# Performance work log

Hardware: AMD Instinct MI355X
Metric: run time of the kernel (lower is better)

Reference implementation:

```python
import jax, jax.numpy as jnp
import numpy as np

V = 25   # NTU joints
NE = 5   # number of hyper-edge types


def setup_inputs() -> dict:
    key = jax.random.key(0)
    ks = jax.random.split(key, 8)
    N, C, T = 64, 12, 300
    x = jax.random.normal(ks[0], (N, C, T, V), dtype=jnp.float32)
    # binary incidence matrices [V, E] with E == V, as in the NTU hyper-edge tables
    hs = [jax.random.bernoulli(ks[1 + i], 0.2, (V, V)).astype(jnp.float32) for i in range(NE)]
    in_ch, out_ch = 3, 64
    w_mlp = jax.random.normal(ks[6], (out_ch, in_ch * NE), dtype=jnp.float32) * (1.0 / np.sqrt(in_ch * NE))
    b_mlp = jnp.zeros((out_ch,), dtype=jnp.float32)
    return {"x": x, "h_local": hs[0], "h_center": hs[1], "h_figl": hs[2],
            "h_figr": hs[3], "h_hand": hs[4], "w_mlp": w_mlp, "b_mlp": b_mlp}


def _normalized_aggregate(w, h):
    # w: [N, T, E], h: [V, E] (E == V)
    degree_v = jnp.einsum('ve,bte->btv', h, w)
    # pow(d, -0.5): inf at d==0 and nan at d<0 are both zeroed in the original
    dv_pos = degree_v > 0
    degree_v = jnp.where(dv_pos, jax.lax.rsqrt(jnp.where(dv_pos, degree_v, 1.0)), 0.0)
    degree_e = jnp.sum(h, axis=0)                      # [E]
    de_nz = degree_e != 0
    degree_e = jnp.where(de_nz, 1.0 / jnp.where(de_nz, degree_e, 1.0), 0.0)
    # fused dh * w * degree_e chain: [N, T, V, E]
    dhwb = degree_v[..., None] * h[None, None] * w[:, :, None, :] * degree_e
    dhwbht = jnp.einsum('btve,ue->btvu', dhwb, h)      # [N, T, V, V]
    return dhwbht * degree_v[:, :, None, :]


def reference(x, h_local, h_center, h_figl, h_figr, h_hand, w_mlp, b_mlp):
    ws = (x[:, 6], x[:, 7], x[:, 9], x[:, 10], x[:, 11])
    hs = (h_local, h_center, h_figl, h_figr, h_hand)
    hwh_cat = jnp.concatenate([_normalized_aggregate(w, h) for w, h in zip(ws, hs)], axis=-2)  # [N,T,5V,V]
    feat = x[:, :3]                                    # [N, 3, T, V]
    N, C, T, Vv = feat.shape
    support = jnp.einsum('btvu,bctu->bctv', hwh_cat, feat)          # [N, C, T, 5V]
    support = support.reshape(N, C, T, NE, Vv).transpose(0, 3, 1, 2, 4).reshape(N, NE * C, T, Vv)
    out = jnp.einsum('oi,bitv->botv', w_mlp, support) + b_mlp[None, :, None, None]
    return jax.nn.relu(out)
```

## Files before the change

### kernel.cpp

```cpp
#include <hip/hip_runtime.h>

#define NE  5
#define V   25
#define NT  300
#define NC  12
#define CO  64
#define WPB 4
#define GX  38
#define WOFF 384

typedef float f4 __attribute__((ext_vector_type(4)));
typedef float f2 __attribute__((ext_vector_type(2)));

#define WSYNC() do { asm volatile("s_waitcnt lgkmcnt(0)" ::: "memory"); \
                     __builtin_amdgcn_sched_barrier(0); } while (0)

__device__ __forceinline__ float hsel(unsigned m, int e, float w) {
    int s = ((int)(m << (31 - e))) >> 31;
    return __int_as_float(__float_as_int(w) & s);
}

#define ODV  0
#define OFP  250
#define OE_  1000
#define OFT  1250
#define OB_  1400
#define OST  1000
#define SCRF 2152

__global__ void setup_kernel(const float* __restrict__ h0, const float* __restrict__ h1,
                             const float* __restrict__ h2, const float* __restrict__ h3,
                             const float* __restrict__ h4,
                             const float* __restrict__ wmlp, const float* __restrict__ bmlp,
                             unsigned* __restrict__ ws) {
    int tid = threadIdx.x;
    float* wsf = (float*)ws;
    if (tid < 125) {
        int i = tid / 25, v = tid % 25;
        const float* hp = (i==0)?h0:(i==1)?h1:(i==2)?h2:(i==3)?h3:h4;
        unsigned m = 0;
        for (int e = 0; e < V; ++e) if (hp[v*V + e] != 0.f) m |= (1u << e);
        ws[tid] = m;
    } else if (tid < 250) {
        int idx = tid - 125, i = idx / 25, e = idx % 25;
        const float* hp = (i==0)?h0:(i==1)?h1:(i==2)?h2:(i==3)?h3:h4;
        unsigned m = 0; float s = 0.f;
        for (int u = 0; u < V; ++u) {
            float hv = hp[u*V + e];
            s += hv;
            if (hv != 0.f) m |= (1u << u);
        }
        ws[tid] = m;
        wsf[125 + tid] = (s != 0.f) ? __fdiv_rn(1.f, s) : 0.f;
    }
    for (int q = tid; q < CO*16; q += 384) {
        int o = q >> 4, k = q & 15;
        wsf[WOFF + q] = (k < 15) ? wmlp[o*15 + k] : bmlp[o];
    }
}

__global__ __launch_bounds__(256, 4) void hyper_main(
    const float* __restrict__ x,
    const unsigned* __restrict__ ws,
    float* __restrict__ out)
{
    __shared__ unsigned RM[125];
    __shared__ unsigned CM[125];
    __shared__ float    DE[125];
    __shared__ __align__(16) float SCR[WPB][SCRF];

    const int tid  = threadIdx.x;
    const int lane = tid & 63;
    const int wid  = tid >> 6;
    const int b    = blockIdx.y;
    const float* wsf = (const float*)ws;

    if (tid < 125) {
        RM[tid] = ws[tid];
    } else if (tid < 250) {
        CM[tid - 125] = ws[tid];
        DE[tid - 125] = wsf[tid + 125];
    }
    __syncthreads();

    const int pp = blockIdx.x * WPB + wid;
    if (pp >= NT/2) return;

    float* S = SCR[wid];

    float pf[7]; int lo[7];
    #pragma unroll
    for (int r = 0; r < 7; ++r) {
        int q  = r*64 + lane;
        int qq = (q < 400) ? q : 0;
        int tt = qq / 200, rr = qq % 200, ch = rr / 25, e = rr % 25;
        int xc = (ch < 5) ? (ch + 6 + (ch >= 2 ? 1 : 0)) : (ch - 5);
        lo[r] = ((ch < 5) ? (OE_ + tt*125 + ch*25) : (OFT + tt*75 + (ch-5)*25)) + e;
        pf[r] = x[((size_t)(b*NC + xc)*NT + (2*pp + tt))*V + e];
    }
    #pragma unroll
    for (int r = 0; r < 6; ++r) S[lo[r]] = pf[r];
    if (lane < 16) S[lo[6]] = pf[6];
    WSYNC();

    #pragma unroll
    for (int r = 0; r < 4; ++r) {
        int idx = r*64 + lane;
        if (idx < 250) {
            int tt  = (idx >= 125) ? 1 : 0;
            int rem = idx - (tt ? 125 : 0);
            int i = rem / 25, v = rem % 25;
            unsigned m = RM[rem];
            const float* wi = S + OE_ + tt*125 + i*25;
            float L0 = 0.f, L1 = 0.f, L2 = 0.f, L3 = 0.f;
            unsigned mm;
            mm = m & 0x00111111u;
            while (mm) { int e = __builtin_ctz(mm); mm &= mm-1; L0 = __fadd_rn(L0, wi[e]); }
            mm = m & 0x00222222u;
            while (mm) { int e = __builtin_ctz(mm); mm &= mm-1; L1 = __fadd_rn(L1, wi[e]); }
            mm = m & 0x00444444u;
            while (mm) { int e = __builtin_ctz(mm); mm &= mm-1; L2 = __fadd_rn(L2, wi[e]); }
            mm = m & 0x00888888u;
            while (mm) { int e = __builtin_ctz(mm); mm &= mm-1; L3 = __fadd_rn(L3, wi[e]); }
            float s = __fadd_rn(__fadd_rn(L0, L1), __fadd_rn(L2, L3));
            s = __fadd_rn(s, hsel(m, 24, wi[24]));
            float dvv = (s > 0.f) ? (float)(1.0 / sqrt((double)s)) : 0.f;
            S[ODV + tt*125 + i*25 + v] = dvv;
            float f0  = S[OFT + tt*75 +  0 + v];
            float f1  = S[OFT + tt*75 + 25 + v];
            float f2v = S[OFT + tt*75 + 50 + v];
            S[OB_ + tt*375 +   0 + i*25 + v] = dvv * f0;
            S[OB_ + tt*375 + 125 + i*25 + v] = dvv * f1;
            S[OB_ + tt*375 + 250 + i*25 + v] = dvv * f2v;
        }
    }
    WSYNC();

    #pragma unroll
    for (int r = 0; r < 4; ++r) {
        int idx = r*64 + lane;
        if (idx < 250) {
            int tt  = (idx >= 125) ? 1 : 0;
            int rem = idx - (tt ? 125 : 0);
            int i = rem / 25, e = rem % 25;
            unsigned m = CM[rem];
            const float* bp = S + OB_ + tt*375 + i*25;
            float a0 = 0.f, a1 = 0.f, a2 = 0.f;
            while (m) {
                int u = __builtin_ctz(m); m &= m - 1;
                a0 += bp[u]; a1 += bp[125 + u]; a2 += bp[250 + u];
            }
            float gg = S[OE_ + tt*125 + i*25 + e] * DE[rem];
            S[OFP + tt*375 + (i*3+0)*25 + e] = a0 * gg;
            S[OFP + tt*375 + (i*3+1)*25 + e] = a1 * gg;
            S[OFP + tt*375 + (i*3+2)*25 + e] = a2 * gg;
        }
    }
    WSYNC();

    #pragma unroll
    for (int r = 0; r < 4; ++r) {
        int idx = r*64 + lane;
        if (idx < 250) {
            int tt  = (idx >= 125) ? 1 : 0;
            int rem = idx - (tt ? 125 : 0);
            int i = rem / 25, v = rem % 25;
            unsigned m = RM[rem];
            const float* fp = S + OFP + tt*375 + i*3*25;
            float a0 = 0.f, a1 = 0.f, a2 = 0.f;
            while (m) {
                int e = __builtin_ctz(m); m &= m - 1;
                a0 += fp[e]; a1 += fp[25 + e]; a2 += fp[50 + e];
            }
            float dd = S[ODV + tt*125 + i*25 + v];
            float* st = S + OST + (tt*25 + v)*20 + i*3;
            st[0] = a0 * dd; st[1] = a1 * dd; st[2] = a2 * dd;
        }
    }
    WSYNC();

    if (lane < 50) {
        const float* st = S + OST + lane*20;
        f4 s0 = *(const f4*)(st+0), s1 = *(const f4*)(st+4),
           s2 = *(const f4*)(st+8), s3 = *(const f4*)(st+12);
        float* ob = out + (size_t)b*CO*7500 + (size_t)pp*50 + lane;
        const f4* wq = (const f4*)(wsf + WOFF);
        #pragma unroll 4
        for (int o = 0; o < CO; ++o) {
            f4 c0 = wq[4*o+0], c1 = wq[4*o+1], c2 = wq[4*o+2], c3 = wq[4*o+3];
            f2 acc = (f2){c3.w, 0.f};
            acc += (f2){c0.x, c0.y} * (f2){s0.x, s0.y};
            acc += (f2){c0.z, c0.w} * (f2){s0.z, s0.w};
            acc += (f2){c1.x, c1.y} * (f2){s1.x, s1.y};
            acc += (f2){c1.z, c1.w} * (f2){s1.z, s1.w};
            acc += (f2){c2.x, c2.y} * (f2){s2.x, s2.y};
            acc += (f2){c2.z, c2.w} * (f2){s2.z, s2.w};
            acc += (f2){c3.x, c3.y} * (f2){s3.x, s3.y};
            float res = acc.x + __fmaf_rn(c3.z, s3.z, acc.y);
            __builtin_nontemporal_store(fmaxf(res, 0.f), ob + (size_t)o*7500);
        }
    }
}

extern "C" void kernel_launch(void* const* d_in, const int* in_sizes, int n_in,
                              void* d_out, int out_size, void* d_ws, size_t ws_size,
                              hipStream_t stream) {
    const float* x    = (const float*)d_in[0];
    const float* h0   = (const float*)d_in[1];
    const float* h1   = (const float*)d_in[2];
    const float* h2   = (const float*)d_in[3];
    const float* h3   = (const float*)d_in[4];
    const float* h4   = (const float*)d_in[5];
    const float* wmlp = (const float*)d_in[6];
    const float* bmlp = (const float*)d_in[7];
    float* out = (float*)d_out;
    unsigned* wsm = (unsigned*)d_ws;

    setup_kernel<<<dim3(1,1,1), dim3(384,1,1), 0, stream>>>(
        h0, h1, h2, h3, h4, wmlp, bmlp, wsm);
    hyper_main<<<dim3(GX, 64, 1), dim3(256,1,1), 0, stream>>>(x, wsm, out);
}
```

Before: 83.35 us.

## Split fused kernel into aggregation and MLP kernels via workspace staging

The single fused kernel becomes two. The aggregation kernel now handles one timestep per wavefront instead of two, which halves shared memory per wave and raises the occupancy target to 8. It writes the 15-channel support, padded to 16, into a global staging buffer. A separate MLP kernel reads that buffer with all 256 threads active and writes the 64 output channels. Before, only 50 of 64 lanes did the MLP and store phase. The cost is an extra global write and read of the staged support (about 30 MB) plus one more kernel launch.

```diff
diff --git a/kernel.cpp b/kernel.cpp
--- a/kernel.cpp
+++ b/kernel.cpp
@@ -5,9 +5,8 @@
 #define NT  300
 #define NC  12
 #define CO  64
-#define WPB 4
-#define GX  38
 #define WOFF 384
+#define STOFF 2048
 
 typedef float f4 __attribute__((ext_vector_type(4)));
 typedef float f2 __attribute__((ext_vector_type(2)));
@@ -21,12 +20,12 @@
 }
 
 #define ODV  0
-#define OFP  250
-#define OE_  1000
-#define OFT  1250
-#define OB_  1400
-#define OST  1000
-#define SCRF 2152
+#define OFP  125
+#define OE_  500
+#define OFT  625
+#define OB_  700
+#define OST  500
+#define SCRF 1088
 
 __global__ void setup_kernel(const float* __restrict__ h0, const float* __restrict__ h1,
                              const float* __restrict__ h2, const float* __restrict__ h3,
@@ -59,15 +58,15 @@
     }
 }
 
-__global__ __launch_bounds__(256, 4) void hyper_main(
+__global__ __launch_bounds__(256, 8) void hyper_agg(
     const float* __restrict__ x,
     const unsigned* __restrict__ ws,
-    float* __restrict__ out)
+    float* __restrict__ wsf_out)
 {
     __shared__ unsigned RM[125];
     __shared__ unsigned CM[125];
     __shared__ float    DE[125];
-    __shared__ __align__(16) float SCR[WPB][SCRF];
+    __shared__ __align__(16) float SCR[4][SCRF];
 
     const int tid  = threadIdx.x;
     const int lane = tid & 63;
@@ -83,35 +82,28 @@
     }
     __syncthreads();
 
-    const int pp = blockIdx.x * WPB + wid;
-    if (pp >= NT/2) return;
-
+    const int t = blockIdx.x * 4 + wid;
     float* S = SCR[wid];
 
-    float pf[7]; int lo[7];
-    #pragma unroll
-    for (int r = 0; r < 7; ++r) {
-        int q  = r*64 + lane;
-        int qq = (q < 400) ? q : 0;
-        int tt = qq / 200, rr = qq % 200, ch = rr / 25, e = rr % 25;
-        int xc = (ch < 5) ? (ch + 6 + (ch >= 2 ? 1 : 0)) : (ch - 5);
-        lo[r] = ((ch < 5) ? (OE_ + tt*125 + ch*25) : (OFT + tt*75 + (ch-5)*25)) + e;
-        pf[r] = x[((size_t)(b*NC + xc)*NT + (2*pp + tt))*V + e];
-    }
-    #pragma unroll
-    for (int r = 0; r < 6; ++r) S[lo[r]] = pf[r];
-    if (lane < 16) S[lo[6]] = pf[6];
-    WSYNC();
-
     #pragma unroll
     for (int r = 0; r < 4; ++r) {
+        int q = r*64 + lane;
+        if (q < 200) {
+            int ch = q / 25, e = q % 25;
+            int xc = (ch < 5) ? (ch + 6 + (ch >= 2 ? 1 : 0)) : (ch - 5);
+            int o = (ch < 5) ? (OE_ + ch*25 + e) : (OFT + (ch-5)*25 + e);
+            S[o] = x[((size_t)(b*NC + xc)*NT + t)*V + e];
+        }
+    }
+    WSYNC();
+
+    #pragma unroll
+    for (int r = 0; r < 2; ++r) {
         int idx = r*64 + lane;
-        if (idx < 250) {
-            int tt  = (idx >= 125) ? 1 : 0;
-            int rem = idx - (tt ? 125 : 0);
-            int i = rem / 25, v = rem % 25;
-            unsigned m = RM[rem];
-            const float* wi = S + OE_ + tt*125 + i*25;
+        if (idx < 125) {
+            int i = idx / 25, v = idx % 25;
+            unsigned m = RM[idx];
+            const float* wi = S + OE_ + i*25;
             float L0 = 0.f, L1 = 0.f, L2 = 0.f, L3 = 0.f;
             unsigned mm;
             mm = m & 0x00111111u;
@@ -125,80 +117,93 @@
             float s = __fadd_rn(__fadd_rn(L0, L1), __fadd_rn(L2, L3));
             s = __fadd_rn(s, hsel(m, 24, wi[24]));
             float dvv = (s > 0.f) ? (float)(1.0 / sqrt((double)s)) : 0.f;
-            S[ODV + tt*125 + i*25 + v] = dvv;
-            float f0  = S[OFT + tt*75 +  0 + v];
-            float f1  = S[OFT + tt*75 + 25 + v];
-            float f2v = S[OFT + tt*75 + 50 + v];
-            S[OB_ + tt*375 +   0 + i*25 + v] = dvv * f0;
-            S[OB_ + tt*375 + 125 + i*25 + v] = dvv * f1;
-            S[OB_ + tt*375 + 250 + i*25 + v] = dvv * f2v;
-        }
-    }
-    WSYNC();
-
-    #pragma unroll
-    for (int r = 0; r < 4; ++r) {
+            S[ODV + i*25 + v] = dvv;
+            S[OB_ +   0 + i*25 + v] = dvv * S[OFT +  0 + v];
+            S[OB_ + 125 + i*25 + v] = dvv * S[OFT + 25 + v];
+            S[OB_ + 250 + i*25 + v] = dvv * S[OFT + 50 + v];
+        }
+    }
+    WSYNC();
+
+    #pragma unroll
+    for (int r = 0; r < 2; ++r) {
         int idx = r*64 + lane;
-        if (idx < 250) {
-            int tt  = (idx >= 125) ? 1 : 0;
-            int rem = idx - (tt ? 125 : 0);
-            int i = rem / 25, e = rem % 25;
-            unsigned m = CM[rem];
-            const float* bp = S + OB_ + tt*375 + i*25;
+        if (idx < 125) {
+            int i = idx / 25, e = idx % 25;
+            unsigned m = CM[idx];
+            const float* bp = S + OB_ + i*25;
             float a0 = 0.f, a1 = 0.f, a2 = 0.f;
             while (m) {
                 int u = __builtin_ctz(m); m &= m - 1;
                 a0 += bp[u]; a1 += bp[125 + u]; a2 += bp[250 + u];
             }
-            float gg = S[OE_ + tt*125 + i*25 + e] * DE[rem];
-            S[OFP + tt*375 + (i*3+0)*25 + e] = a0 * gg;
-            S[OFP + tt*375 + (i*3+1)*25 + e] = a1 * gg;
-            S[OFP + tt*375 + (i*3+2)*25 + e] = a2 * gg;
-        }
-    }
-    WSYNC();
-
-    #pragma unroll
-    for (int r = 0; r < 4; ++r) {
+            float gg = S[OE_ + i*25 + e] * DE[idx];
+            S[OFP + (i*3+0)*25 + e] = a0 * gg;
+            S[OFP + (i*3+1)*25 + e] = a1 * gg;
+            S[OFP + (i*3+2)*25 + e] = a2 * gg;
+        }
+    }
+    WSYNC();
+
+    #pragma unroll
+    for (int r = 0; r < 3; ++r) {
         int idx = r*64 + lane;
-        if (idx < 250) {
-            int tt  = (idx >= 125) ? 1 : 0;
-            int rem = idx - (tt ? 125 : 0);
-            int i = rem / 25, v = rem % 25;
-            unsigned m = RM[rem];
-            const float* fp = S + OFP + tt*375 + i*3*25;
+        if (idx < 125) {
+            int i = idx / 25, v = idx % 25;
+            unsigned m = RM[idx];
+            const float* fp = S + OFP + i*3*25;
             float a0 = 0.f, a1 = 0.f, a2 = 0.f;
             while (m) {
                 int e = __builtin_ctz(m); m &= m - 1;
                 a0 += fp[e]; a1 += fp[25 + e]; a2 += fp[50 + e];
             }
-            float dd = S[ODV + tt*125 + i*25 + v];
-            float* st = S + OST + (tt*25 + v)*20 + i*3;
+            float dd = S[ODV + i*25 + v];
+            float* st = S + OST + v*16 + i*3;
             st[0] = a0 * dd; st[1] = a1 * dd; st[2] = a2 * dd;
-        }
-    }
-    WSYNC();
-
-    if (lane < 50) {
-        const float* st = S + OST + lane*20;
-        f4 s0 = *(const f4*)(st+0), s1 = *(const f4*)(st+4),
-           s2 = *(const f4*)(st+8), s3 = *(const f4*)(st+12);
-        float* ob = out + (size_t)b*CO*7500 + (size_t)pp*50 + lane;
-        const f4* wq = (const f4*)(wsf + WOFF);
-        #pragma unroll 4
-        for (int o = 0; o < CO; ++o) {
-            f4 c0 = wq[4*o+0], c1 = wq[4*o+1], c2 = wq[4*o+2], c3 = wq[4*o+3];
-            f2 acc = (f2){c3.w, 0.f};
-            acc += (f2){c0.x, c0.y} * (f2){s0.x, s0.y};
-            acc += (f2){c0.z, c0.w} * (f2){s0.z, s0.w};
-            acc += (f2){c1.x, c1.y} * (f2){s1.x, s1.y};
-            acc += (f2){c1.z, c1.w} * (f2){s1.z, s1.w};
-            acc += (f2){c2.x, c2.y} * (f2){s2.x, s2.y};
-            acc += (f2){c2.z, c2.w} * (f2){s2.z, s2.w};
-            acc += (f2){c3.x, c3.y} * (f2){s3.x, s3.y};
-            float res = acc.x + __fmaf_rn(c3.z, s3.z, acc.y);
-            __builtin_nontemporal_store(fmaxf(res, 0.f), ob + (size_t)o*7500);
-        }
+        } else if (idx < 150) {
+            S[OST + (idx - 125)*16 + 15] = 0.f;
+        }
+    }
+    WSYNC();
+
+    if (lane < 25) {
+        const f4* sr = (const f4*)(S + OST + lane*16);
+        f4 r0 = sr[0], r1 = sr[1], r2 = sr[2], r3 = sr[3];
+        f4* stg = (f4*)(wsf_out + STOFF) + ((size_t)b*7500 + t*25 + lane)*4;
+        __builtin_nontemporal_store(r0, stg + 0);
+        __builtin_nontemporal_store(r1, stg + 1);
+        __builtin_nontemporal_store(r2, stg + 2);
+        __builtin_nontemporal_store(r3, stg + 3);
+    }
+}
+
+__global__ __launch_bounds__(256, 8) void hyper_mlp(
+    const unsigned* __restrict__ ws,
+    float* __restrict__ out)
+{
+    const float* wsf = (const float*)ws;
+    const int p = blockIdx.x * 256 + threadIdx.x;
+    if (p >= 7500) return;
+    const int b = blockIdx.y;
+
+    const f4* sp = (const f4*)(wsf + STOFF) + ((size_t)b*7500 + p)*4;
+    f4 s0 = sp[0], s1 = sp[1], s2 = sp[2], s3 = sp[3];
+
+    float* ob = out + (size_t)b*CO*7500 + p;
+    const f4* wq = (const f4*)(wsf + WOFF);
+    #pragma unroll 4
+    for (int o = 0; o < CO; ++o) {
+        f4 c0 = wq[4*o+0], c1 = wq[4*o+1], c2 = wq[4*o+2], c3 = wq[4*o+3];
+        f2 acc = (f2){c3.w, 0.f};
+        acc += (f2){c0.x, c0.y} * (f2){s0.x, s0.y};
+        acc += (f2){c0.z, c0.w} * (f2){s0.z, s0.w};
+        acc += (f2){c1.x, c1.y} * (f2){s1.x, s1.y};
+        acc += (f2){c1.z, c1.w} * (f2){s1.z, s1.w};
+        acc += (f2){c2.x, c2.y} * (f2){s2.x, s2.y};
+        acc += (f2){c2.z, c2.w} * (f2){s2.z, s2.w};
+        acc += (f2){c3.x, c3.y} * (f2){s3.x, s3.y};
+        float res = acc.x + __fmaf_rn(c3.z, s3.z, acc.y);
+        __builtin_nontemporal_store(fmaxf(res, 0.f), ob + (size_t)o*7500);
     }
 }
 
@@ -218,5 +223,8 @@
 
     setup_kernel<<<dim3(1,1,1), dim3(384,1,1), 0, stream>>>(
         h0, h1, h2, h3, h4, wmlp, bmlp, wsm);
-    hyper_main<<<dim3(GX, 64, 1), dim3(256,1,1), 0, stream>>>(x, wsm, out);
-}
+    hyper_agg<<<dim3(75, 64, 1), dim3(256,1,1), 0, stream>>>(
+        x, wsm, (float*)d_ws);
+    hyper_mlp<<<dim3(30, 64, 1), dim3(256,1,1), 0, stream>>>(
+        wsm, out);
+}
```

Result: slower. 92.65 us (+11.2%).
